# Kernel optimization log

Hardware: AMD Instinct MI355X
Metric: run time of the kernel (lower is better)

The kernel has to match this reference:

```python
import jax, jax.numpy as jnp
import numpy as np

T, B, IN, HID, OUT = 512, 2048, 28, 198, 10

def setup_inputs() -> dict:
    key = jax.random.key(0)
    ks = jax.random.split(key, 6)
    s = 1.0 / np.sqrt(HID)
    return {
        "x": jax.random.normal(ks[0], (T, B, IN), dtype=jnp.float32),
        "H": jax.random.normal(ks[1], (HID, HID), dtype=jnp.float32) * s,
        "U": jax.random.normal(ks[2], (IN, HID), dtype=jnp.float32) * s,
        "A": jax.random.normal(ks[3], (OUT, HID), dtype=jnp.float32) * s,
        "b": jax.random.normal(ks[4], (HID,), dtype=jnp.float32) * 0.1,
        "c": jax.random.normal(ks[5], (OUT,), dtype=jnp.float32) * 0.1,
    }

def reference(x, H, U, A, b, c):
    # Precompute input projections for all timesteps in one big GEMM:
    # [T,B,IN] @ [IN,HID] -> [T,B,HID]
    xu = jnp.einsum('tbi,ih->tbh', x, U) + b

    def step(h, xu_t):
        h = jnp.tanh(h @ H.T + xu_t)
        return h, None

    h0 = jnp.zeros((x.shape[1], H.shape[0]), dtype=x.dtype)
    h, _ = jax.lax.scan(step, h0, xu)
    return h @ A.T + c
```

## Files before the change

### kernel.cpp

```cpp
#include <hip/hip_runtime.h>


#define T_STEPS 512
#define BATCH   2048
#define IN_DIM  28
#define HID     198
#define OUT_DIM 10
#define BB      8
#define KT      8
#define NCW     13

typedef __attribute__((ext_vector_type(8))) _Float16 half8;
typedef __attribute__((ext_vector_type(4))) float   floatx4;

__device__ __forceinline__ floatx4 mfma16(half8 a, half8 b, floatx4 c) {
    return __builtin_amdgcn_mfma_f32_16x16x32_f16(a, b, c, 0, 0, 0);
}

__device__ __forceinline__ float fast_tanh(float x) {
    float e = __builtin_amdgcn_exp2f(x * 2.885390081777926357f);
    float r = __builtin_amdgcn_rcpf(e + 1.0f);
    return __builtin_fmaf(-2.0f, r, 1.0f);
}

__global__ void __launch_bounds__(1024, 4)
rnn_kernel(const float* __restrict__ x, const float* __restrict__ H,
           const float* __restrict__ U, const float* __restrict__ A,
           const float* __restrict__ bvec, const float* __restrict__ cvec,
           float* __restrict__ out)
{
    __shared__ __align__(16) _Float16 lds_A[2][KT][32][8];
    __shared__ float lds_h[BB][204];

    const int tid  = threadIdx.x;
    const int lane = tid & 63;
    const int wv   = tid >> 6;
    const int m    = lane & 15;
    const int quad = lane >> 4;
    const int r8   = m & 7;
    const int b0   = blockIdx.x * BB;

    {
        _Float16* p0 = &lds_A[0][0][0][0];
        for (int i = tid; i < 2*KT*32*8; i += 1024) p0[i] = (_Float16)0.0f;
    }
    __syncthreads();

    floatx4 zero4 = {0.0f, 0.0f, 0.0f, 0.0f};

    half8 Bf[KT];
    float bias_eff = 0.0f;
    int   jcol = 0, e_ktd = 0, e_chunk8 = 0, e_idx = 0;
    bool  e_wr = false;
    if (wv < NCW) {
        jcol = wv*16 + m;
        bias_eff = (jcol < HID) ? bvec[jcol] : 0.0f;
        #pragma unroll
        for (int kt = 0; kt < 7; ++kt) {
            half8 f;
            #pragma unroll
            for (int idx = 0; idx < 8; ++idx) {
                int k = kt*32 + quad*8 + idx;
                float v = (jcol < HID && k < HID) ? H[jcol*HID + k] : 0.0f;
                f[idx] = (_Float16)v;
            }
            Bf[kt] = f;
        }
        {
            half8 f;
            #pragma unroll
            for (int idx = 0; idx < 8; ++idx) {
                int i = quad*8 + idx;
                float v = (jcol < HID && i < IN_DIM) ? U[i*HID + jcol] : 0.0f;
                f[idx] = (_Float16)v;
            }
            Bf[7] = f;
        }
        e_ktd    = jcol >> 5;
        e_chunk8 = ((jcol & 31) >> 3) * 8;
        e_idx    = jcol & 7;
        e_wr     = (jcol < HID);
    }

    const int regbase = (quad >> 1) * 2;
    const int rowbase = (quad & 1) * 4 + regbase;

    const int srow  = lane & 31;
    const int sq    = srow >> 3;
    const int sr8   = srow & 7;
    const float* xrow_s = x + (size_t)(b0 + sr8) * IN_DIM + sq*8;
    const size_t tstride = (size_t)BATCH * IN_DIM;

    auto stage = [&](int tn, int buf) {
        if (lane < 32) {
            const float* p = xrow_s + (size_t)tn * tstride;
            floatx4 f0 = *(const floatx4*)p;
            floatx4 f1 = (sq < 3) ? *(const floatx4*)(p + 4) : zero4;
            half8 ax;
            ax[0] = (_Float16)f0[0]; ax[1] = (_Float16)f0[1];
            ax[2] = (_Float16)f0[2]; ax[3] = (_Float16)f0[3];
            ax[4] = (_Float16)f1[0]; ax[5] = (_Float16)f1[1];
            ax[6] = (_Float16)f1[2]; ax[7] = (_Float16)f1[3];
            *(half8*)&lds_A[buf][7][srow][0] = ax;
        }
    };

    if (wv == 15) stage(0, 0);

    #pragma unroll 1
    for (int t = 0; t < T_STEPS; ++t) {
        const int rb = t & 1;
        const int wb = rb ^ 1;

        __syncthreads();

        if (wv < NCW) {
            floatx4 acc1 = (floatx4){bias_eff, bias_eff, bias_eff, bias_eff};
            floatx4 acc2 = zero4;
            #pragma unroll
            for (int kt = 0; kt < KT; ++kt) {
                half8 a = *(const half8*)&lds_A[rb][kt][quad*8 + r8][0];
                if (kt & 1) acc2 = mfma16(a, Bf[kt], acc2);
                else        acc1 = mfma16(a, Bf[kt], acc1);
            }
            if (e_wr) {
                #pragma unroll
                for (int e = 0; e < 2; ++e) {
                    const int reg = regbase + e;
                    const int row = (quad & 1) * 4 + reg;
                    float v = fast_tanh(acc1[reg] + acc2[reg]);
                    lds_A[wb][e_ktd][e_chunk8 + row][e_idx] = (_Float16)v;
                    if (t == T_STEPS - 1) lds_h[row][jcol] = v;
                }
            }
        } else if (wv == 15) {
            const int tn = (t + 1 < T_STEPS) ? (t + 1) : t;
            stage(tn, wb);
        }
    }

    __syncthreads();

    if (tid < BB * OUT_DIM) {
        const int r = tid / OUT_DIM;
        const int o = tid % OUT_DIM;
        float s = cvec[o];
        for (int k = 0; k < HID; ++k) s += lds_h[r][k] * A[o*HID + k];
        out[(size_t)(b0 + r) * OUT_DIM + o] = s;
    }
}

extern "C" void kernel_launch(void* const* d_in, const int* in_sizes, int n_in,
                              void* d_out, int out_size, void* d_ws, size_t ws_size,
                              hipStream_t stream) {
    const float* x  = (const float*)d_in[0];
    const float* H  = (const float*)d_in[1];
    const float* U  = (const float*)d_in[2];
    const float* A  = (const float*)d_in[3];
    const float* b  = (const float*)d_in[4];
    const float* c  = (const float*)d_in[5];
    float* out = (float*)d_out;

    rnn_kernel<<<dim3(BATCH / BB), dim3(1024), 0, stream>>>(x, H, U, A, b, c, out);
}
```

Before: 452.1 us.

## Halve block size with two column tiles per wave and register-prefetched x

Shrinks the block from 1024 to 512 threads. Five 'heavy' waves each compute two 16-column MFMA tiles and three waves compute one, so the 13 tiles are spread over 8 waves. The x staging wave now issues global loads two steps ahead into registers and commits them to LDS, which hides load latency from the per-step barrier. The time loop is unrolled by two with fixed buffer indices. The goal is cheaper per-step __syncthreads with fewer waves and less x-load stall, at the cost of more register pressure and longer per-wave MFMA chains.

After: 508.0 us. 12.4% more time.

```diff
diff --git a/kernel.cpp b/kernel.cpp
--- a/kernel.cpp
+++ b/kernel.cpp
@@ -8,7 +8,7 @@
 #define OUT_DIM 10
 #define BB      8
 #define KT      8
-#define NCW     13
+#define NTHREADS 512
 
 typedef __attribute__((ext_vector_type(8))) _Float16 half8;
 typedef __attribute__((ext_vector_type(4))) float   floatx4;
@@ -23,7 +23,7 @@
     return __builtin_fmaf(-2.0f, r, 1.0f);
 }
 
-__global__ void __launch_bounds__(1024, 4)
+__global__ void __launch_bounds__(NTHREADS, 1)
 rnn_kernel(const float* __restrict__ x, const float* __restrict__ H,
            const float* __restrict__ U, const float* __restrict__ A,
            const float* __restrict__ bvec, const float* __restrict__ cvec,
@@ -39,104 +39,125 @@
     const int quad = lane >> 4;
     const int r8   = m & 7;
     const int b0   = blockIdx.x * BB;
+    const bool heavy = (wv < 5);
 
     {
         _Float16* p0 = &lds_A[0][0][0][0];
-        for (int i = tid; i < 2*KT*32*8; i += 1024) p0[i] = (_Float16)0.0f;
+        for (int i = tid; i < 2*KT*32*8; i += NTHREADS) p0[i] = (_Float16)0.0f;
     }
+
+    const floatx4 zero4 = {0.0f, 0.0f, 0.0f, 0.0f};
+
+    const int jcolA = wv*16 + m;
+    const int jcolB = jcolA + 128;
+    const bool bReal = heavy && (jcolB < HID);
+    const float biasA = bvec[jcolA];
+    const float biasB = bReal ? bvec[jcolB] : 0.0f;
+
+    half8 BfA[KT], BfB[KT];
+    #pragma unroll
+    for (int kt = 0; kt < 7; ++kt) {
+        half8 fa, fb;
+        #pragma unroll
+        for (int idx = 0; idx < 8; ++idx) {
+            const int k = kt*32 + quad*8 + idx;
+            fa[idx] = (_Float16)((k < HID) ? H[jcolA*HID + k] : 0.0f);
+            fb[idx] = (_Float16)((bReal && k < HID) ? H[jcolB*HID + k] : 0.0f);
+        }
+        BfA[kt] = fa; BfB[kt] = fb;
+    }
+    {
+        half8 fa, fb;
+        #pragma unroll
+        for (int idx = 0; idx < 8; ++idx) {
+            const int i = quad*8 + idx;
+            fa[idx] = (_Float16)((i < IN_DIM) ? U[i*HID + jcolA] : 0.0f);
+            fb[idx] = (_Float16)((bReal && i < IN_DIM) ? U[i*HID + jcolB] : 0.0f);
+        }
+        BfA[7] = fa; BfB[7] = fb;
+    }
+
+    const int eA_ktd = jcolA >> 5, eA_c8 = ((jcolA & 31) >> 3)*8, eA_idx = jcolA & 7;
+    const int eB_ktd = jcolB >> 5, eB_c8 = ((jcolB & 31) >> 3)*8, eB_idx = jcolB & 7;
+    const int regbase = (quad >> 1) * 2;
+
+    const int srow = lane & 31, sq = srow >> 3, sr8 = srow & 7;
+    const float* xrow_s = x + (size_t)(b0 + sr8) * IN_DIM + sq*8;
+    const size_t tstride = (size_t)BATCH * IN_DIM;
+    floatx4 sA0 = zero4, sA1 = zero4, sB0 = zero4, sB1 = zero4;
+
+    auto issueLd = [&](int tn, floatx4& f0, floatx4& f1) {
+        const float* p = xrow_s + (size_t)tn * tstride;
+        f0 = *(const floatx4*)p;
+        f1 = (sq < 3) ? *(const floatx4*)(p + 4) : zero4;
+    };
+    auto commitX = [&](floatx4 f0, floatx4 f1, int buf) {
+        half8 ax;
+        ax[0] = (_Float16)f0[0]; ax[1] = (_Float16)f0[1];
+        ax[2] = (_Float16)f0[2]; ax[3] = (_Float16)f0[3];
+        ax[4] = (_Float16)f1[0]; ax[5] = (_Float16)f1[1];
+        ax[6] = (_Float16)f1[2]; ax[7] = (_Float16)f1[3];
+        *(half8*)&lds_A[buf][7][srow][0] = ax;
+    };
+
     __syncthreads();
 
-    floatx4 zero4 = {0.0f, 0.0f, 0.0f, 0.0f};
-
-    half8 Bf[KT];
-    float bias_eff = 0.0f;
-    int   jcol = 0, e_ktd = 0, e_chunk8 = 0, e_idx = 0;
-    bool  e_wr = false;
-    if (wv < NCW) {
-        jcol = wv*16 + m;
-        bias_eff = (jcol < HID) ? bvec[jcol] : 0.0f;
-        #pragma unroll
-        for (int kt = 0; kt < 7; ++kt) {
-            half8 f;
-            #pragma unroll
-            for (int idx = 0; idx < 8; ++idx) {
-                int k = kt*32 + quad*8 + idx;
-                float v = (jcol < HID && k < HID) ? H[jcol*HID + k] : 0.0f;
-                f[idx] = (_Float16)v;
-            }
-            Bf[kt] = f;
-        }
-        {
-            half8 f;
-            #pragma unroll
-            for (int idx = 0; idx < 8; ++idx) {
-                int i = quad*8 + idx;
-                float v = (jcol < HID && i < IN_DIM) ? U[i*HID + jcol] : 0.0f;
-                f[idx] = (_Float16)v;
-            }
-            Bf[7] = f;
-        }
-        e_ktd    = jcol >> 5;
-        e_chunk8 = ((jcol & 31) >> 3) * 8;
-        e_idx    = jcol & 7;
-        e_wr     = (jcol < HID);
+    if (wv == 5 && lane < 32) {
+        floatx4 t0, t1;
+        issueLd(0, t0, t1);
+        issueLd(1, sA0, sA1);
+        issueLd(2, sB0, sB1);
+        commitX(t0, t1, 0);
     }
 
-    const int regbase = (quad >> 1) * 2;
-    const int rowbase = (quad & 1) * 4 + regbase;
-
-    const int srow  = lane & 31;
-    const int sq    = srow >> 3;
-    const int sr8   = srow & 7;
-    const float* xrow_s = x + (size_t)(b0 + sr8) * IN_DIM + sq*8;
-    const size_t tstride = (size_t)BATCH * IN_DIM;
-
-    auto stage = [&](int tn, int buf) {
-        if (lane < 32) {
-            const float* p = xrow_s + (size_t)tn * tstride;
-            floatx4 f0 = *(const floatx4*)p;
-            floatx4 f1 = (sq < 3) ? *(const floatx4*)(p + 4) : zero4;
-            half8 ax;
-            ax[0] = (_Float16)f0[0]; ax[1] = (_Float16)f0[1];
-            ax[2] = (_Float16)f0[2]; ax[3] = (_Float16)f0[3];
-            ax[4] = (_Float16)f1[0]; ax[5] = (_Float16)f1[1];
-            ax[6] = (_Float16)f1[2]; ax[7] = (_Float16)f1[3];
-            *(half8*)&lds_A[buf][7][srow][0] = ax;
+    auto computeStep = [&](int rb, int wb, bool last) {
+        floatx4 aA1 = {biasA, biasA, biasA, biasA};
+        floatx4 aA2 = zero4;
+        floatx4 aB1 = {biasB, biasB, biasB, biasB};
+        floatx4 aB2 = zero4;
+        #pragma unroll
+        for (int kt = 0; kt < KT; ++kt) {
+            const half8 av = *(const half8*)&lds_A[rb][kt][quad*8 + r8][0];
+            if (kt & 1) {
+                aA2 = mfma16(av, BfA[kt], aA2);
+                if (heavy) aB2 = mfma16(av, BfB[kt], aB2);
+            } else {
+                aA1 = mfma16(av, BfA[kt], aA1);
+                if (heavy) aB1 = mfma16(av, BfB[kt], aB1);
+            }
+        }
+        #pragma unroll
+        for (int e = 0; e < 2; ++e) {
+            const int reg = regbase + e;
+            const int row = (quad & 1)*4 + reg;
+            const float vA = fast_tanh(aA1[reg] + aA2[reg]);
+            lds_A[wb][eA_ktd][eA_c8 + row][eA_idx] = (_Float16)vA;
+            if (last) lds_h[row][jcolA] = vA;
+            if (bReal) {
+                const float vB = fast_tanh(aB1[reg] + aB2[reg]);
+                lds_A[wb][eB_ktd][eB_c8 + row][eB_idx] = (_Float16)vB;
+                if (last) lds_h[row][jcolB] = vB;
+            }
         }
     };
 
-    if (wv == 15) stage(0, 0);
-
     #pragma unroll 1
-    for (int t = 0; t < T_STEPS; ++t) {
-        const int rb = t & 1;
-        const int wb = rb ^ 1;
+    for (int t = 0; t < T_STEPS; t += 2) {
+        __syncthreads();
+        if (wv == 5 && lane < 32) {
+            commitX(sA0, sA1, 1);
+            const int tn = (t+3 < T_STEPS) ? (t+3) : (T_STEPS-1);
+            issueLd(tn, sA0, sA1);
+        }
+        computeStep(0, 1, false);
 
         __syncthreads();
-
-        if (wv < NCW) {
-            floatx4 acc1 = (floatx4){bias_eff, bias_eff, bias_eff, bias_eff};
-            floatx4 acc2 = zero4;
-            #pragma unroll
-            for (int kt = 0; kt < KT; ++kt) {
-                half8 a = *(const half8*)&lds_A[rb][kt][quad*8 + r8][0];
-                if (kt & 1) acc2 = mfma16(a, Bf[kt], acc2);
-                else        acc1 = mfma16(a, Bf[kt], acc1);
-            }
-            if (e_wr) {
-                #pragma unroll
-                for (int e = 0; e < 2; ++e) {
-                    const int reg = regbase + e;
-                    const int row = (quad & 1) * 4 + reg;
-                    float v = fast_tanh(acc1[reg] + acc2[reg]);
-                    lds_A[wb][e_ktd][e_chunk8 + row][e_idx] = (_Float16)v;
-                    if (t == T_STEPS - 1) lds_h[row][jcol] = v;
-                }
-            }
-        } else if (wv == 15) {
-            const int tn = (t + 1 < T_STEPS) ? (t + 1) : t;
-            stage(tn, wb);
+        if (wv == 5 && lane < 32) {
+            commitX(sB0, sB1, 0);
+            const int tn = (t+4 < T_STEPS) ? (t+4) : (T_STEPS-1);
+            issueLd(tn, sB0, sB1);
         }
+        computeStep(1, 0, (t + 2) == T_STEPS);
     }
 
     __syncthreads();
@@ -161,5 +182,5 @@
     const float* c  = (const float*)d_in[5];
     float* out = (float*)d_out;
 
-    rnn_kernel<<<dim3(BATCH / BB), dim3(1024), 0, stream>>>(x, H, U, A, b, c, out);
+    rnn_kernel<<<dim3(BATCH / BB), dim3(NTHREADS), 0, stream>>>(x, H, U, A, b, c, out);
 }
```
